# Optimization experiments

Measured on AMD Instinct MI355X. Metric: run time of the kernel, lower is better.

Reference implementation:

```python
import jax, jax.numpy as jnp
import numpy as np

# Static problem dims (match input_specs / init_kwargs)
B, NQ, C, H = 2, 900, 256, 8
HGT, WID = 64, 64            # single-scale feature map (input_spatial_shapes = [[64, 64]])
N = HGT * WID                # 4096 keys
DH = C // H                  # head dim 32
RPE_HID = 512
STRIDE = 16                  # feature_stride


def setup_inputs() -> dict:
    key = jax.random.key(0)
    ks = jax.random.split(key, 24)
    p = lambda k, shape: jax.random.normal(k, shape, jnp.float32) * 0.02
    # reference boxes (cx, cy, w, h) in pixel coords of a 1024x1024 image
    ref = jax.random.uniform(ks[0], (B, NQ, 1, 4), jnp.float32)
    ref = jnp.concatenate([ref[..., :2] * (WID * STRIDE), ref[..., 2:] * 128.0], axis=-1)
    return {
        "vggt_features": jnp.zeros((1,), jnp.float32),  # unused by forward (kept for signature fidelity)
        "query": jax.random.normal(ks[1], (B, NQ, C), jnp.float32),
        "reference_2d": ref,
        "k_input_flatten": jax.random.normal(ks[2], (B, N, C), jnp.float32),
        "v_input_flatten": jax.random.normal(ks[3], (B, N, C), jnp.float32),
        "input_spatial_shapes": jnp.array([[HGT, WID]], jnp.int32),
        "input_padding_mask": jnp.zeros((B, N), jnp.bool_),
        # cpb_mlp1 (x) and cpb_mlp2 (y): Linear(2,512)+ReLU+Linear(512,H,no bias); stored as [in,out]
        "W1x": p(ks[4], (2, RPE_HID)), "b1x": jnp.zeros((RPE_HID,), jnp.float32), "W2x": p(ks[5], (RPE_HID, H)),
        "W1y": p(ks[6], (2, RPE_HID)), "b1y": jnp.zeros((RPE_HID,), jnp.float32), "W2y": p(ks[7], (RPE_HID, H)),
        "Wq": p(ks[8], (C, C)), "bq": jnp.zeros((C,), jnp.float32),
        "Wk": p(ks[9], (C, C)), "bk": jnp.zeros((C,), jnp.float32),
        "Wv": p(ks[10], (C, C)), "bv": jnp.zeros((C,), jnp.float32),
        "Wp": p(ks[11], (C, C)), "bp": jnp.zeros((C,), jnp.float32),
    }


def _mlp(d, W1, b1, W2):
    return jax.nn.relu(d @ W1 + b1) @ W2


def reference(vggt_features, query, reference_2d, k_input_flatten, v_input_flatten,
              input_spatial_shapes, input_padding_mask,
              W1x, b1x, W2x, W1y, b1y, W2y, Wq, bq, Wk, bk, Wv, bv, Wp, bp):
    h, w = HGT, WID  # static (input_spatial_shapes[0] == [HGT, WID])
    scale = DH ** -0.5
    # cxcywh -> xyxy: [B, NQ, 1, 4]
    xyxy = jnp.concatenate([reference_2d[..., :2] - reference_2d[..., 2:] / 2,
                            reference_2d[..., :2] + reference_2d[..., 2:] / 2], axis=-1)
    # pixel-center grid coords (linspace(0.5, w-0.5, w) * stride)
    pos_x = ((jnp.arange(w, dtype=jnp.float32) + 0.5) * STRIDE)[None, None, :, None]
    pos_y = ((jnp.arange(h, dtype=jnp.float32) + 0.5) * STRIDE)[None, None, :, None]
    delta_x = xyxy[..., 0::2] - pos_x  # [B, NQ, w, 2]  (x1, x2 rel. to columns)
    delta_y = xyxy[..., 1::2] - pos_y  # [B, NQ, h, 2]  (y1, y2 rel. to rows)
    rpe_x = _mlp(delta_x, W1x, b1x, W2x)  # [B, NQ, w, H]
    rpe_y = _mlp(delta_y, W1y, b1y, W2y)  # [B, NQ, h, H]
    # broadcast add over (row, col) then flatten spatial -> [B, H, NQ, N]
    rpe = (rpe_x[:, :, None] + rpe_y[:, :, :, None]).reshape(B, NQ, h * w, H).transpose(0, 3, 1, 2)
    q = (query @ Wq + bq).reshape(B, NQ, H, DH).transpose(0, 2, 1, 3) * scale  # [B,H,NQ,DH]
    k = (k_input_flatten @ Wk + bk).reshape(B, N, H, DH).transpose(0, 2, 1, 3)  # [B,H,N,DH]
    v = (v_input_flatten @ Wv + bv).reshape(B, N, H, DH).transpose(0, 2, 1, 3)  # [B,H,N,DH]
    attn = jnp.einsum('bhqd,bhkd->bhqk', q, k) + rpe
    attn = attn + input_padding_mask[:, None, None, :].astype(attn.dtype) * (-100.0)
    # torch.clip_ to finfo(min,max) is an identity on finite values; softmax follows
    attn = jax.nn.softmax(attn, axis=-1)
    x = jnp.einsum('bhqk,bhkd->bhqd', attn, v).transpose(0, 2, 1, 3).reshape(B, NQ, C)
    return x @ Wp + bp
```

## Files before the change

kernel.cpp:

```cpp
#include <hip/hip_runtime.h>
#include <hip/hip_bf16.h>
#include <cmath>

#define B_ 2
#define NQ_ 900
#define N_ 4096
#define LOG2E 1.4426950408889634f

typedef __attribute__((ext_vector_type(4))) float f32x4;
typedef __attribute__((ext_vector_type(8))) short s16x8;
typedef __attribute__((ext_vector_type(8))) _Float16 f16x8;

__device__ inline short f2bf(float x) {
    union { __hip_bfloat16 b; short s; } u;
    u.b = __float2bfloat16(x);
    return u.s;
}
__device__ inline short f2h(float x) {
    _Float16 h = (_Float16)x;
    return __builtin_bit_cast(short, h);
}

template <int CTRL>
__device__ inline float dppf(float x) {
    int xi = __builtin_bit_cast(int, x);
    int r = __builtin_amdgcn_update_dpp(xi, xi, CTRL, 0xF, 0xF, true);
    return __builtin_bit_cast(float, r);
}
__device__ inline float rowmax16(float v) {
    v = fmaxf(v, dppf<0x121>(v));
    v = fmaxf(v, dppf<0x122>(v));
    v = fmaxf(v, dppf<0x124>(v));
    v = fmaxf(v, dppf<0x128>(v));
    return v;
}
__device__ inline float rowsum16(float v) {
    v += dppf<0x121>(v);
    v += dppf<0x122>(v);
    v += dppf<0x124>(v);
    v += dppf<0x128>(v);
    return v;
}

__global__ __launch_bounds__(256) void stage1_kernel(
    const float* __restrict__ query, const float* __restrict__ kin,
    const float* __restrict__ vin,
    const float* __restrict__ Wq, const float* __restrict__ Wk,
    const float* __restrict__ Wv,
    const float* __restrict__ bqv, const float* __restrict__ bkv,
    const float* __restrict__ bvv,
    unsigned short* __restrict__ qbf, unsigned short* __restrict__ kbf,
    unsigned short* __restrict__ vbf, float qscale,
    const float* __restrict__ ref2d,
    const float* __restrict__ W1x, const float* __restrict__ b1x,
    const float* __restrict__ W1y, const float* __restrict__ b1y,
    const float* __restrict__ W2x, const float* __restrict__ W2y,
    float* __restrict__ rpe_x, float* __restrict__ rpe_y)
{
    __shared__ uint4 smem[3072];
    const int bx = blockIdx.x;
    const int tid = threadIdx.x;
    const int w = tid >> 6, l = tid & 63, quad = l >> 4, l15 = l & 15;

    if (bx < 285) {
        short* Ab = (short*)smem;
        short* Bb = (short*)smem + 16384;
        const int mtx = bx < 29 ? 0 : (bx < 157 ? 1 : 2);
        const int tile = bx - (mtx == 0 ? 0 : mtx == 1 ? 29 : 157);
        const int m0 = tile * 64;
        const float* X = mtx == 0 ? query : mtx == 1 ? kin : vin;
        const float* W = mtx == 0 ? Wq : mtx == 1 ? Wk : Wv;
        const float* bias = mtx == 0 ? bqv : mtx == 1 ? bkv : bvv;
        unsigned short* Y = mtx == 0 ? qbf : mtx == 1 ? kbf : vbf;
        const int M = mtx == 0 ? 1800 : 8192;
        const float alpha = mtx == 0 ? qscale : 1.0f;
        const int rows_per_b = mtx == 0 ? 900 : 4096;
        const int ROWS = mtx == 0 ? 960 : 4096;
        const int wq = tid & 3, mm = tid >> 2;

        {
            const bool valid = (m0 + mm) < M;
            const float* xr = X + (size_t)(m0 + mm) * 256;
            #pragma unroll
            for (int it = 0; it < 8; ++it) {
                int g2 = it * 4 + wq;
                float4 a0 = make_float4(0.f, 0.f, 0.f, 0.f), a1 = a0;
                if (valid) {
                    a0 = *(const float4*)(xr + g2 * 8);
                    a1 = *(const float4*)(xr + g2 * 8 + 4);
                }
                uint4 pk;
                pk.x = (unsigned)(unsigned short)f2bf(a0.x) | ((unsigned)(unsigned short)f2bf(a0.y) << 16);
                pk.y = (unsigned)(unsigned short)f2bf(a0.z) | ((unsigned)(unsigned short)f2bf(a0.w) << 16);
                pk.z = (unsigned)(unsigned short)f2bf(a1.x) | ((unsigned)(unsigned short)f2bf(a1.y) << 16);
                pk.w = (unsigned)(unsigned short)f2bf(a1.z) | ((unsigned)(unsigned short)f2bf(a1.w) << 16);
                *(uint4*)(Ab + (it * 256 + mm * 4 + wq) * 8) = pk;
            }
        }

        for (int nt0 = 0; nt0 < 4; ++nt0) {
            const int n0 = nt0 * 64;
            f32x4 acc[4] = {{0.f,0.f,0.f,0.f},{0.f,0.f,0.f,0.f},{0.f,0.f,0.f,0.f},{0.f,0.f,0.f,0.f}};
            for (int kh = 0; kh < 2; ++kh) {
                {
                    const float* wcol = W + n0 + mm;
                    #pragma unroll
                    for (int it = 0; it < 4; ++it) {
                        int g2 = it * 4 + wq;
                        int kb = kh * 128 + g2 * 8;
                        uint4 wk4;
                        wk4.x = (unsigned)(unsigned short)f2bf(wcol[(kb + 0) * 256])
                              | ((unsigned)(unsigned short)f2bf(wcol[(kb + 1) * 256]) << 16);
                        wk4.y = (unsigned)(unsigned short)f2bf(wcol[(kb + 2) * 256])
                              | ((unsigned)(unsigned short)f2bf(wcol[(kb + 3) * 256]) << 16);
                        wk4.z = (unsigned)(unsigned short)f2bf(wcol[(kb + 4) * 256])
                              | ((unsigned)(unsigned short)f2bf(wcol[(kb + 5) * 256]) << 16);
                        wk4.w = (unsigned)(unsigned short)f2bf(wcol[(kb + 6) * 256])
                              | ((unsigned)(unsigned short)f2bf(wcol[(kb + 7) * 256]) << 16);
                        *(uint4*)(Bb + (it * 256 + mm * 4 + wq) * 8) = wk4;
                    }
                }
                __syncthreads();

                #pragma unroll
                for (int kc = 0; kc < 4; ++kc) {
                    int kcg = kh * 4 + kc;
                    s16x8 a = *(const s16x8*)(Ab + (kcg * 256 + (w * 16 + l15) * 4 + quad) * 8);
                    #pragma unroll
                    for (int nt = 0; nt < 4; ++nt) {
                        s16x8 bf = *(const s16x8*)(Bb + (kc * 256 + (nt * 16 + l15) * 4 + quad) * 8);
                        acc[nt] = __builtin_amdgcn_mfma_f32_16x16x32_bf16(a, bf, acc[nt], 0, 0, 0);
                    }
                }
                __syncthreads();
            }

            #pragma unroll
            for (int nt = 0; nt < 4; ++nt) {
                int n = n0 + nt * 16 + l15;
                float bs = bias[n];
                int h = n >> 5, d = n & 31;
                #pragma unroll
                for (int r = 0; r < 4; ++r) {
                    int row = m0 + w * 16 + quad * 4 + r;
                    if (row < M) {
                        int b = row / rows_per_b;
                        int pos = row - b * rows_per_b;
                        Y[((size_t)(b * 8 + h) * ROWS + pos) * 32 + d] =
                            (unsigned short)f2bf((acc[nt][r] + bs) * alpha);
                    }
                }
            }
        }
    } else {
        short* sw2h = (short*)smem;
        short* sw2l = (short*)smem + 8192;
        float4* sUV = (float4*)(smem + 2048);
        const int bq = bx - 285;

        for (int i = tid; i < 8192; i += 256) {
            int g = i >> 3, j = i & 7;
            int kcg = g >> 6, rr = g & 63, n = rr >> 2, q4 = rr & 3;
            int k = kcg * 32 + q4 * 8 + j;
            float val = ((n < 8) ? W2x[k * 8 + n] : W2y[k * 8 + (n - 8)]) * LOG2E;
            _Float16 hi = (_Float16)val;
            sw2h[i] = __builtin_bit_cast(short, hi);
            sw2l[i] = f2h(val - (float)hi);
        }
        for (int k = tid; k < 512; k += 256) {
            float w1x0 = W1x[k], w1x1 = W1x[512 + k];
            float w1y0 = W1y[k], w1y1 = W1y[512 + k];
            float bxv = b1x[k], byv = b1y[k];
            float vx = -(w1x0 + w1x1), vy = -(w1y0 + w1y1);
            const float4 bb = *(const float4*)(ref2d + (size_t)bq * 4);
            float ux = fmaf(w1x0, bb.x - bb.z * 0.5f, fmaf(w1x1, bb.x + bb.z * 0.5f, bxv));
            float uy = fmaf(w1y0, bb.y - bb.w * 0.5f, fmaf(w1y1, bb.y + bb.w * 0.5f, byv));
            sUV[(k >> 3) * 9 + (k & 7)] = make_float4(ux, vx, uy, vy);
        }

        const int wrow = w;
        const int row = wrow * 16 + l15;
        const float pc = (row + 0.5f) * 16.0f;

        __syncthreads();

        f32x4 accx = {0.f, 0.f, 0.f, 0.f}, accy = {0.f, 0.f, 0.f, 0.f};
        for (int kc = 0; kc < 16; ++kc) {
            f16x8 axh, axl, ayh, ayl;
            #pragma unroll
            for (int i = 0; i < 8; ++i) {
                float4 u = sUV[(kc * 4 + quad) * 9 + i];
                float hx = fmaxf(fmaf(u.y, pc, u.x), 0.f);
                float hy = fmaxf(fmaf(u.w, pc, u.z), 0.f);
                _Float16 xh = (_Float16)hx;
                _Float16 yh = (_Float16)hy;
                axh[i] = xh;
                axl[i] = (_Float16)(hx - (float)xh);
                ayh[i] = yh;
                ayl[i] = (_Float16)(hy - (float)yh);
            }
            f16x8 bh = *(const f16x8*)(sw2h + (kc * 64 + l15 * 4 + quad) * 8);
            f16x8 bl = *(const f16x8*)(sw2l + (kc * 64 + l15 * 4 + quad) * 8);
            accx = __builtin_amdgcn_mfma_f32_16x16x32_f16(axh, bh, accx, 0, 0, 0);
            accx = __builtin_amdgcn_mfma_f32_16x16x32_f16(axh, bl, accx, 0, 0, 0);
            accx = __builtin_amdgcn_mfma_f32_16x16x32_f16(axl, bh, accx, 0, 0, 0);
            accy = __builtin_amdgcn_mfma_f32_16x16x32_f16(ayh, bh, accy, 0, 0, 0);
            accy = __builtin_amdgcn_mfma_f32_16x16x32_f16(ayh, bl, accy, 0, 0, 0);
            accy = __builtin_amdgcn_mfma_f32_16x16x32_f16(ayl, bh, accy, 0, 0, 0);
        }

        #pragma unroll
        for (int rr = 0; rr < 4; ++rr) {
            int row_out = wrow * 16 + quad * 4 + rr;
            if (l15 < 8) rpe_x[((size_t)l15 * 1800 + bq) * 64 + row_out] = accx[rr];
            else         rpe_y[((size_t)(l15 - 8) * 1800 + bq) * 64 + row_out] = accy[rr];
        }
    }
}

__global__ __launch_bounds__(256) void outproj_kernel(
    const float* __restrict__ X, const float* __restrict__ W,
    const float* __restrict__ bias, float* __restrict__ Y, int M)
{
    __shared__ short Abh[4096], Abl[4096], Bbh[4096], Bbl[4096];
    const int tid = threadIdx.x;
    const int m0 = blockIdx.x * 64, n0 = blockIdx.y * 64;
    const int w = tid >> 6, l = tid & 63, quad = l >> 4, l15 = l & 15;
    const int wq = tid & 3, mm = tid >> 2;
    const bool valid = (m0 + mm) < M;
    const float* xr = X + (size_t)(m0 + mm) * 256;
    const float* wcol = W + n0 + mm;

    f32x4 acc[4] = {{0.f,0.f,0.f,0.f},{0.f,0.f,0.f,0.f},{0.f,0.f,0.f,0.f},{0.f,0.f,0.f,0.f}};

    for (int kq = 0; kq < 4; ++kq) {
        #pragma unroll
        for (int it = 0; it < 2; ++it) {
            int g2 = it * 4 + wq;
            int kbase = kq * 64 + g2 * 8;
            float av[8], bv[8];
            #pragma unroll
            for (int j = 0; j < 8; ++j) {
                av[j] = valid ? xr[kbase + j] : 0.f;
                bv[j] = wcol[(kbase + j) * 256];
            }
            uint4 ah, al, bh, bl;
            unsigned* ahp = (unsigned*)&ah; unsigned* alp = (unsigned*)&al;
            unsigned* bhp = (unsigned*)&bh; unsigned* blp = (unsigned*)&bl;
            #pragma unroll
            for (int j2 = 0; j2 < 4; ++j2) {
                _Float16 h0 = (_Float16)av[j2 * 2], h1 = (_Float16)av[j2 * 2 + 1];
                ahp[j2] = (unsigned)(unsigned short)__builtin_bit_cast(short, h0)
                        | ((unsigned)(unsigned short)__builtin_bit_cast(short, h1) << 16);
                alp[j2] = (unsigned)(unsigned short)f2h(av[j2 * 2] - (float)h0)
                        | ((unsigned)(unsigned short)f2h(av[j2 * 2 + 1] - (float)h1) << 16);
                _Float16 g0 = (_Float16)bv[j2 * 2], g1 = (_Float16)bv[j2 * 2 + 1];
                bhp[j2] = (unsigned)(unsigned short)__builtin_bit_cast(short, g0)
                        | ((unsigned)(unsigned short)__builtin_bit_cast(short, g1) << 16);
                blp[j2] = (unsigned)(unsigned short)f2h(bv[j2 * 2] - (float)g0)
                        | ((unsigned)(unsigned short)f2h(bv[j2 * 2 + 1] - (float)g1) << 16);
            }
            int gi = (it * 256 + mm * 4 + wq) * 8;
            *(uint4*)(Abh + gi) = ah;
            *(uint4*)(Abl + gi) = al;
            *(uint4*)(Bbh + gi) = bh;
            *(uint4*)(Bbl + gi) = bl;
        }
        __syncthreads();

        #pragma unroll
        for (int kc = 0; kc < 2; ++kc) {
            int ga = (kc * 256 + (w * 16 + l15) * 4 + quad) * 8;
            f16x8 ah = *(const f16x8*)(Abh + ga);
            f16x8 al = *(const f16x8*)(Abl + ga);
            #pragma unroll
            for (int nt = 0; nt < 4; ++nt) {
                int gb = (kc * 256 + (nt * 16 + l15) * 4 + quad) * 8;
                f16x8 bh = *(const f16x8*)(Bbh + gb);
                f16x8 bl = *(const f16x8*)(Bbl + gb);
                acc[nt] = __builtin_amdgcn_mfma_f32_16x16x32_f16(ah, bh, acc[nt], 0, 0, 0);
                acc[nt] = __builtin_amdgcn_mfma_f32_16x16x32_f16(ah, bl, acc[nt], 0, 0, 0);
                acc[nt] = __builtin_amdgcn_mfma_f32_16x16x32_f16(al, bh, acc[nt], 0, 0, 0);
            }
        }
        __syncthreads();
    }

    #pragma unroll
    for (int nt = 0; nt < 4; ++nt) {
        int n = n0 + nt * 16 + l15;
        float bs = bias[n];
        #pragma unroll
        for (int r = 0; r < 4; ++r) {
            int row = m0 + w * 16 + quad * 4 + r;
            if (row < M)
                Y[(size_t)row * 256 + n] = acc[nt][r] + bs;
        }
    }
}

__global__ __launch_bounds__(512, 4) void attn_mfma_kernel(
    const unsigned short* __restrict__ qb16, const unsigned short* __restrict__ kb16,
    const unsigned short* __restrict__ vb16,
    const float* __restrict__ rpe_x, const float* __restrict__ rpe_y,
    const unsigned char* __restrict__ mask, float* __restrict__ xout)
{
    __shared__ short skf[4 * 2048];
    __shared__ short svt[4 * 2048];
    __shared__ short spb[8 * 544];
    __shared__ float ry[32 * 65];
    __shared__ unsigned long long smaskb[64];
    __shared__ float sm[8][16], sl[8][16], sLf[32];

    const int tid = threadIdx.x;
    const int qb = blockIdx.x, h = blockIdx.y, b = blockIdx.z;
    const int q0 = qb * 32;
    const int w = tid >> 6, l = tid & 63;
    const int qsub = w >> 2, g = w & 3;
    const int quad = l >> 4, l15 = l & 15;

    const unsigned short* qg = qb16 + (size_t)(b * 8 + h) * 960 * 32;
    const unsigned short* kg = kb16 + (size_t)(b * 8 + h) * 4096 * 32;
    const unsigned short* vg = vb16 + (size_t)(b * 8 + h) * 4096 * 32;
    const float* rxh = rpe_x + ((size_t)h * 1800 + b * NQ_) * 64;
    const float* ryh = rpe_y + ((size_t)h * 1800 + b * NQ_) * 64;

    for (int i = tid; i < 2048; i += 512) {
        int qq = q0 + (i >> 6), pos = i & 63;
        float vy = 0.f;
        if (qq < NQ_)
            vy = ryh[(size_t)qq * 64 + pos];
        ry[(i >> 6) * 65 + pos] = vy;
    }
    #pragma unroll
    for (int j = 0; j < 8; ++j) {
        int c = w * 8 + j;
        unsigned long long bits = __ballot(mask[(size_t)b * N_ + c * 64 + l] != 0);
        if (l == 0) smaskb[c] = bits;
    }

    s16x8 qa = *(const s16x8*)(qg + (size_t)(q0 + qsub * 16 + l15) * 32 + quad * 8);

    f32x4 rx4[4];
    #pragma unroll
    for (int t = 0; t < 4; ++t)
        #pragma unroll
        for (int r = 0; r < 4; ++r) {
            int qq = q0 + qsub * 16 + quad * 4 + r;
            rx4[t][r] = (qq < NQ_) ? rxh[(size_t)qq * 64 + t * 16 + l15] : 0.f;
        }

    const int sg = tid >> 7, role = (tid >> 6) & 1, stl = tid & 63;
    int eoff[4];
    if (role == 0) {
        #pragma unroll
        for (int t = 0; t < 4; ++t)
            eoff[t] = (t * 16 + (stl & 15)) * 32 + (stl >> 4) * 8;
    } else {
        #pragma unroll
        for (int t = 0; t < 4; ++t)
            eoff[t] = stl * 32 + t * 8;
    }
    const unsigned short* src = role ? vg : kg;

    uint4 pf[4];
    {
        size_t cb = (size_t)(sg * 16) * 2048;
        #pragma unroll
        for (int t = 0; t < 4; ++t) pf[t] = *(const uint4*)(src + cb + eoff[t]);
    }

    float mrow[4] = {-INFINITY, -INFINITY, -INFINITY, -INFINITY};
    float lrow[4] = {0.f, 0.f, 0.f, 0.f};
    f32x4 acc0 = {0.f, 0.f, 0.f, 0.f}, acc1 = {0.f, 0.f, 0.f, 0.f};
    short* pw = spb + w * 544;

    for (int i = 0; i < 16; ++i) {
        __syncthreads();
        if (role == 0) {
            #pragma unroll
            for (int t = 0; t < 4; ++t)
                *(uint4*)(skf + sg * 2048 + (t * 64 + stl) * 8) = pf[t];
        } else {
            short* vtw = svt + sg * 2048;
            #pragma unroll
            for (int t = 0; t < 4; ++t) {
                const unsigned short* pv = (const unsigned short*)&pf[t];
                #pragma unroll
                for (int j = 0; j < 8; ++j) {
                    int d = t * 8 + j;
                    vtw[d * 64 + (((stl >> 3) ^ (d & 7)) << 3) + (stl & 7)] = (short)pv[j];
                }
            }
        }
        __syncthreads();

        {
            int inext = (i + 1 < 16) ? i + 1 : 15;
            size_t cb = (size_t)(sg * 16 + inext) * 2048;
            #pragma unroll
            for (int t = 0; t < 4; ++t) pf[t] = *(const uint4*)(src + cb + eoff[t]);
        }

        const int cgc = g * 16 + i;
        const short* kf = skf + g * 2048;

        f32x4 sc[4];
        #pragma unroll
        for (int t = 0; t < 4; ++t) {
            s16x8 kb = *(const s16x8*)(kf + (t * 64 + l) * 8);
            sc[t] = __builtin_amdgcn_mfma_f32_16x16x32_bf16(qa, kb, rx4[t], 0, 0, 0);
        }
        float ryv[4];
        #pragma unroll
        for (int r = 0; r < 4; ++r)
            ryv[r] = ry[(qsub * 16 + quad * 4 + r) * 65 + cgc];
        unsigned long long mb = smaskb[cgc];
        if (mb) {
            #pragma unroll
            for (int t = 0; t < 4; ++t) {
                float mk = ((mb >> (t * 16 + l15)) & 1ULL) ? -144.2695f : 0.f;
                #pragma unroll
                for (int r = 0; r < 4; ++r) sc[t][r] += mk;
            }
        }

        float cmr[4];
        #pragma unroll
        for (int r = 0; r < 4; ++r)
            cmr[r] = fmaxf(fmaxf(sc[0][r], sc[1][r]), fmaxf(sc[2][r], sc[3][r])) + ryv[r];

        int ok = (cmr[0] <= mrow[0] + 8.f) & (cmr[1] <= mrow[1] + 8.f)
               & (cmr[2] <= mrow[2] + 8.f) & (cmr[3] <= mrow[3] + 8.f);
        if (!__all(ok)) {
            #pragma unroll
            for (int r = 0; r < 4; ++r) {
                float cm = rowmax16(cmr[r]);
                float mnew = fmaxf(mrow[r], cm);
                float al = exp2f(mrow[r] - mnew);
                mrow[r] = mnew;
                lrow[r] *= al;
                acc0[r] *= al;
                acc1[r] *= al;
            }
        }

        float msub[4];
        #pragma unroll
        for (int r = 0; r < 4; ++r) msub[r] = mrow[r] - ryv[r];
        #pragma unroll
        for (int t = 0; t < 4; ++t)
            #pragma unroll
            for (int r = 0; r < 4; ++r)
                sc[t][r] = exp2f(sc[t][r] - msub[r]);
        #pragma unroll
        for (int r = 0; r < 4; ++r)
            lrow[r] += (sc[0][r] + sc[1][r]) + (sc[2][r] + sc[3][r]);

        const short* vt = svt + g * 2048;
        #pragma unroll
        for (int hh = 0; hh < 2; ++hh) {
            #pragma unroll
            for (int tt = 0; tt < 2; ++tt) {
                int t = hh * 2 + tt;
                int gphys = (tt * 2 + (l15 >> 3)) ^ quad;
                #pragma unroll
                for (int r = 0; r < 4; ++r)
                    pw[(gphys * 17 + quad * 4 + r) * 8 + (l15 & 7)] = f2bf(sc[t][r]);
            }
            int gph_r = quad ^ (l15 >> 2);
            s16x8 pa  = *(const s16x8*)(pw + (gph_r * 17 + l15) * 8);
            int ksw = ((hh * 4 + quad) ^ (l15 & 7)) * 8;
            s16x8 vb0 = *(const s16x8*)(vt + l15 * 64 + ksw);
            s16x8 vb1 = *(const s16x8*)(vt + (16 + l15) * 64 + ksw);
            acc0 = __builtin_amdgcn_mfma_f32_16x16x32_bf16(pa, vb0, acc0, 0, 0, 0);
            acc1 = __builtin_amdgcn_mfma_f32_16x16x32_bf16(pa, vb1, acc1, 0, 0, 0);
        }
    }

    #pragma unroll
    for (int r = 0; r < 4; ++r) lrow[r] = rowsum16(lrow[r]);

    __syncthreads();
    if (l15 == 0) {
        #pragma unroll
        for (int r = 0; r < 4; ++r) {
            sm[w][quad * 4 + r] = mrow[r];
            sl[w][quad * 4 + r] = lrow[r];
        }
    }
    __syncthreads();
    float wgt[4], L4[4];
    #pragma unroll
    for (int r = 0; r < 4; ++r) {
        int qrow = quad * 4 + r;
        float mm = -INFINITY;
        #pragma unroll
        for (int gg = 0; gg < 4; ++gg) mm = fmaxf(mm, sm[qsub * 4 + gg][qrow]);
        float LL = 0.f;
        #pragma unroll
        for (int gg = 0; gg < 4; ++gg)
            LL += exp2f(sm[qsub * 4 + gg][qrow] - mm) * sl[qsub * 4 + gg][qrow];
        wgt[r] = exp2f(mrow[r] - mm);
        L4[r] = LL;
    }
    if (g == 0 && l15 == 0) {
        #pragma unroll
        for (int r = 0; r < 4; ++r) sLf[qsub * 16 + quad * 4 + r] = L4[r];
    }

    float* obuf = (float*)skf;
    for (int gg = 0; gg < 4; ++gg) {
        if (g == gg) {
            #pragma unroll
            for (int r = 0; r < 4; ++r) {
                int idx = (qsub * 16 + quad * 4 + r) * 33 + l15;
                float v0 = wgt[r] * acc0[r];
                float v1 = wgt[r] * acc1[r];
                if (gg == 0) { obuf[idx] = v0; obuf[idx + 16] = v1; }
                else         { obuf[idx] += v0; obuf[idx + 16] += v1; }
            }
        }
        __syncthreads();
    }

    for (int i = tid; i < 1024; i += 512) {
        int ql = i >> 5, d = i & 31;
        int qq = q0 + ql;
        if (qq < NQ_)
            xout[(size_t)(b * NQ_ + qq) * 256 + h * 32 + d] = obuf[ql * 33 + d] / sLf[ql];
    }
}

extern "C" void kernel_launch(void* const* d_in, const int* in_sizes, int n_in,
                              void* d_out, int out_size, void* d_ws, size_t ws_size,
                              hipStream_t stream)
{
    const float* query = (const float*)d_in[1];
    const float* ref2d = (const float*)d_in[2];
    const float* kin   = (const float*)d_in[3];
    const float* vin   = (const float*)d_in[4];
    const unsigned char* mask = (const unsigned char*)d_in[6];
    const float* W1x = (const float*)d_in[7];
    const float* b1x = (const float*)d_in[8];
    const float* W2x = (const float*)d_in[9];
    const float* W1y = (const float*)d_in[10];
    const float* b1y = (const float*)d_in[11];
    const float* W2y = (const float*)d_in[12];
    const float* Wq  = (const float*)d_in[13];
    const float* bq  = (const float*)d_in[14];
    const float* Wk  = (const float*)d_in[15];
    const float* bk  = (const float*)d_in[16];
    const float* Wv  = (const float*)d_in[17];
    const float* bv  = (const float*)d_in[18];
    const float* Wp  = (const float*)d_in[19];
    const float* bp  = (const float*)d_in[20];

    char* wsb = (char*)d_ws;
    unsigned short* qbf = (unsigned short*)(wsb);
    unsigned short* kbf = (unsigned short*)(wsb +   983040);
    unsigned short* vbf = (unsigned short*)(wsb +  5177344);
    float* rxws = (float*)(wsb +  9371648);
    float* ryws = (float*)(wsb + 13058048);
    float* xws  = (float*)(wsb + 16744448);
    float* out  = (float*)d_out;

    const float qscale = LOG2E / sqrtf(32.0f);

    stage1_kernel<<<2085, 256, 0, stream>>>(
        query, kin, vin, Wq, Wk, Wv, bq, bk, bv, qbf, kbf, vbf, qscale,
        ref2d, W1x, b1x, W1y, b1y, W2x, W2y, rxws, ryws);
    attn_mfma_kernel<<<dim3(29, 8, B_), 512, 0, stream>>>(
        qbf, kbf, vbf, rxws, ryws, mask, xws);
    outproj_kernel<<<dim3(29, 4), 256, 0, stream>>>(xws, Wp, bp, out, 1800);
}
```

Measured before the change: 218.0 us.

## Keep GEMM A-fragments in registers and batch four queries per RPE block

The projection GEMM path now loads each wave's A rows straight into register fragments instead of staging them in shared memory. The full 256-deep weight slice is staged once per n-tile, which removes the K-half split and one barrier pair. The RPE path processes four queries per block, reusing the staged W2 hi/lo tables and W1 values, so the grid shrinks from 2085 to 735 blocks. The costs are higher register pressure and a serialized per-query loop with extra barriers inside each RPE block.

Measured after the change: 203.9 us. 1.07x faster.

```diff
diff --git a/kernel.cpp b/kernel.cpp
--- a/kernel.cpp
+++ b/kernel.cpp
@@ -57,14 +57,13 @@
     const float* __restrict__ W2x, const float* __restrict__ W2y,
     float* __restrict__ rpe_x, float* __restrict__ rpe_y)
 {
-    __shared__ uint4 smem[3072];
+    __shared__ uint4 smem[2560];
     const int bx = blockIdx.x;
     const int tid = threadIdx.x;
     const int w = tid >> 6, l = tid & 63, quad = l >> 4, l15 = l & 15;
 
     if (bx < 285) {
-        short* Ab = (short*)smem;
-        short* Bb = (short*)smem + 16384;
+        short* Bb = (short*)smem;
         const int mtx = bx < 29 ? 0 : (bx < 157 ? 1 : 2);
         const int tile = bx - (mtx == 0 ? 0 : mtx == 1 ? 29 : 157);
         const int m0 = tile * 64;
@@ -78,61 +77,56 @@
         const int ROWS = mtx == 0 ? 960 : 4096;
         const int wq = tid & 3, mm = tid >> 2;
 
+        s16x8 afr[8];
         {
-            const bool valid = (m0 + mm) < M;
-            const float* xr = X + (size_t)(m0 + mm) * 256;
-            #pragma unroll
-            for (int it = 0; it < 8; ++it) {
-                int g2 = it * 4 + wq;
+            const int arow = m0 + w * 16 + l15;
+            const bool avalid = arow < M;
+            const float* xr = X + (size_t)arow * 256;
+            #pragma unroll
+            for (int kc = 0; kc < 8; ++kc) {
                 float4 a0 = make_float4(0.f, 0.f, 0.f, 0.f), a1 = a0;
-                if (valid) {
-                    a0 = *(const float4*)(xr + g2 * 8);
-                    a1 = *(const float4*)(xr + g2 * 8 + 4);
+                if (avalid) {
+                    a0 = *(const float4*)(xr + kc * 32 + quad * 8);
+                    a1 = *(const float4*)(xr + kc * 32 + quad * 8 + 4);
                 }
-                uint4 pk;
-                pk.x = (unsigned)(unsigned short)f2bf(a0.x) | ((unsigned)(unsigned short)f2bf(a0.y) << 16);
-                pk.y = (unsigned)(unsigned short)f2bf(a0.z) | ((unsigned)(unsigned short)f2bf(a0.w) << 16);
-                pk.z = (unsigned)(unsigned short)f2bf(a1.x) | ((unsigned)(unsigned short)f2bf(a1.y) << 16);
-                pk.w = (unsigned)(unsigned short)f2bf(a1.z) | ((unsigned)(unsigned short)f2bf(a1.w) << 16);
-                *(uint4*)(Ab + (it * 256 + mm * 4 + wq) * 8) = pk;
+                unsigned pk0 = (unsigned)(unsigned short)f2bf(a0.x) | ((unsigned)(unsigned short)f2bf(a0.y) << 16);
+                unsigned pk1 = (unsigned)(unsigned short)f2bf(a0.z) | ((unsigned)(unsigned short)f2bf(a0.w) << 16);
+                unsigned pk2 = (unsigned)(unsigned short)f2bf(a1.x) | ((unsigned)(unsigned short)f2bf(a1.y) << 16);
+                unsigned pk3 = (unsigned)(unsigned short)f2bf(a1.z) | ((unsigned)(unsigned short)f2bf(a1.w) << 16);
+                uint4 pk = make_uint4(pk0, pk1, pk2, pk3);
+                afr[kc] = __builtin_bit_cast(s16x8, pk);
             }
         }
 
         for (int nt0 = 0; nt0 < 4; ++nt0) {
             const int n0 = nt0 * 64;
+            {
+                const float* wcol = W + n0 + mm;
+                #pragma unroll
+                for (int it = 0; it < 8; ++it) {
+                    int g2 = it * 4 + wq;
+                    uint4 wk4;
+                    wk4.x = (unsigned)(unsigned short)f2bf(wcol[(g2 * 8 + 0) * 256])
+                          | ((unsigned)(unsigned short)f2bf(wcol[(g2 * 8 + 1) * 256]) << 16);
+                    wk4.y = (unsigned)(unsigned short)f2bf(wcol[(g2 * 8 + 2) * 256])
+                          | ((unsigned)(unsigned short)f2bf(wcol[(g2 * 8 + 3) * 256]) << 16);
+                    wk4.z = (unsigned)(unsigned short)f2bf(wcol[(g2 * 8 + 4) * 256])
+                          | ((unsigned)(unsigned short)f2bf(wcol[(g2 * 8 + 5) * 256]) << 16);
+                    wk4.w = (unsigned)(unsigned short)f2bf(wcol[(g2 * 8 + 6) * 256])
+                          | ((unsigned)(unsigned short)f2bf(wcol[(g2 * 8 + 7) * 256]) << 16);
+                    *(uint4*)(Bb + (it * 256 + mm * 4 + wq) * 8) = wk4;
+                }
+            }
+            __syncthreads();
+
             f32x4 acc[4] = {{0.f,0.f,0.f,0.f},{0.f,0.f,0.f,0.f},{0.f,0.f,0.f,0.f},{0.f,0.f,0.f,0.f}};
-            for (int kh = 0; kh < 2; ++kh) {
-                {
-                    const float* wcol = W + n0 + mm;
-                    #pragma unroll
-                    for (int it = 0; it < 4; ++it) {
-                        int g2 = it * 4 + wq;
-                        int kb = kh * 128 + g2 * 8;
-                        uint4 wk4;
-                        wk4.x = (unsigned)(unsigned short)f2bf(wcol[(kb + 0) * 256])
-                              | ((unsigned)(unsigned short)f2bf(wcol[(kb + 1) * 256]) << 16);
-                        wk4.y = (unsigned)(unsigned short)f2bf(wcol[(kb + 2) * 256])
-                              | ((unsigned)(unsigned short)f2bf(wcol[(kb + 3) * 256]) << 16);
-                        wk4.z = (unsigned)(unsigned short)f2bf(wcol[(kb + 4) * 256])
-                              | ((unsigned)(unsigned short)f2bf(wcol[(kb + 5) * 256]) << 16);
-                        wk4.w = (unsigned)(unsigned short)f2bf(wcol[(kb + 6) * 256])
-                              | ((unsigned)(unsigned short)f2bf(wcol[(kb + 7) * 256]) << 16);
-                        *(uint4*)(Bb + (it * 256 + mm * 4 + wq) * 8) = wk4;
-                    }
+            #pragma unroll
+            for (int kc = 0; kc < 8; ++kc) {
+                #pragma unroll
+                for (int nt = 0; nt < 4; ++nt) {
+                    s16x8 bf = *(const s16x8*)(Bb + (kc * 256 + (nt * 16 + l15) * 4 + quad) * 8);
+                    acc[nt] = __builtin_amdgcn_mfma_f32_16x16x32_bf16(afr[kc], bf, acc[nt], 0, 0, 0);
                 }
-                __syncthreads();
-
-                #pragma unroll
-                for (int kc = 0; kc < 4; ++kc) {
-                    int kcg = kh * 4 + kc;
-                    s16x8 a = *(const s16x8*)(Ab + (kcg * 256 + (w * 16 + l15) * 4 + quad) * 8);
-                    #pragma unroll
-                    for (int nt = 0; nt < 4; ++nt) {
-                        s16x8 bf = *(const s16x8*)(Bb + (kc * 256 + (nt * 16 + l15) * 4 + quad) * 8);
-                        acc[nt] = __builtin_amdgcn_mfma_f32_16x16x32_bf16(a, bf, acc[nt], 0, 0, 0);
-                    }
-                }
-                __syncthreads();
             }
 
             #pragma unroll
@@ -151,12 +145,13 @@
                     }
                 }
             }
+            __syncthreads();
         }
     } else {
         short* sw2h = (short*)smem;
         short* sw2l = (short*)smem + 8192;
         float4* sUV = (float4*)(smem + 2048);
-        const int bq = bx - 285;
+        const int bq0 = (bx - 285) * 4;
 
         for (int i = tid; i < 8192; i += 256) {
             int g = i >> 3, j = i & 7;
@@ -167,53 +162,66 @@
             sw2h[i] = __builtin_bit_cast(short, hi);
             sw2l[i] = f2h(val - (float)hi);
         }
-        for (int k = tid; k < 512; k += 256) {
-            float w1x0 = W1x[k], w1x1 = W1x[512 + k];
-            float w1y0 = W1y[k], w1y1 = W1y[512 + k];
-            float bxv = b1x[k], byv = b1y[k];
-            float vx = -(w1x0 + w1x1), vy = -(w1y0 + w1y1);
-            const float4 bb = *(const float4*)(ref2d + (size_t)bq * 4);
-            float ux = fmaf(w1x0, bb.x - bb.z * 0.5f, fmaf(w1x1, bb.x + bb.z * 0.5f, bxv));
-            float uy = fmaf(w1y0, bb.y - bb.w * 0.5f, fmaf(w1y1, bb.y + bb.w * 0.5f, byv));
-            sUV[(k >> 3) * 9 + (k & 7)] = make_float4(ux, vx, uy, vy);
-        }
+
+        const int k0 = tid, k1 = tid + 256;
+        const float w1x0a = W1x[k0], w1x1a = W1x[512 + k0];
+        const float w1y0a = W1y[k0], w1y1a = W1y[512 + k0];
+        const float bxa = b1x[k0], bya = b1y[k0];
+        const float vxa = -(w1x0a + w1x1a), vya = -(w1y0a + w1y1a);
+        const float w1x0b = W1x[k1], w1x1b = W1x[512 + k1];
+        const float w1y0b = W1y[k1], w1y1b = W1y[512 + k1];
+        const float bxb = b1x[k1], byb = b1y[k1];
+        const float vxb = -(w1x0b + w1x1b), vyb = -(w1y0b + w1y1b);
 
         const int wrow = w;
         const int row = wrow * 16 + l15;
         const float pc = (row + 0.5f) * 16.0f;
 
-        __syncthreads();
-
-        f32x4 accx = {0.f, 0.f, 0.f, 0.f}, accy = {0.f, 0.f, 0.f, 0.f};
-        for (int kc = 0; kc < 16; ++kc) {
-            f16x8 axh, axl, ayh, ayl;
-            #pragma unroll
-            for (int i = 0; i < 8; ++i) {
-                float4 u = sUV[(kc * 4 + quad) * 9 + i];
-                float hx = fmaxf(fmaf(u.y, pc, u.x), 0.f);
-                float hy = fmaxf(fmaf(u.w, pc, u.z), 0.f);
-                _Float16 xh = (_Float16)hx;
-                _Float16 yh = (_Float16)hy;
-                axh[i] = xh;
-                axl[i] = (_Float16)(hx - (float)xh);
-                ayh[i] = yh;
-                ayl[i] = (_Float16)(hy - (float)yh);
-            }
-            f16x8 bh = *(const f16x8*)(sw2h + (kc * 64 + l15 * 4 + quad) * 8);
-            f16x8 bl = *(const f16x8*)(sw2l + (kc * 64 + l15 * 4 + quad) * 8);
-            accx = __builtin_amdgcn_mfma_f32_16x16x32_f16(axh, bh, accx, 0, 0, 0);
-            accx = __builtin_amdgcn_mfma_f32_16x16x32_f16(axh, bl, accx, 0, 0, 0);
-            accx = __builtin_amdgcn_mfma_f32_16x16x32_f16(axl, bh, accx, 0, 0, 0);
-            accy = __builtin_amdgcn_mfma_f32_16x16x32_f16(ayh, bh, accy, 0, 0, 0);
-            accy = __builtin_amdgcn_mfma_f32_16x16x32_f16(ayh, bl, accy, 0, 0, 0);
-            accy = __builtin_amdgcn_mfma_f32_16x16x32_f16(ayl, bh, accy, 0, 0, 0);
-        }
-
-        #pragma unroll
-        for (int rr = 0; rr < 4; ++rr) {
-            int row_out = wrow * 16 + quad * 4 + rr;
-            if (l15 < 8) rpe_x[((size_t)l15 * 1800 + bq) * 64 + row_out] = accx[rr];
-            else         rpe_y[((size_t)(l15 - 8) * 1800 + bq) * 64 + row_out] = accy[rr];
+        for (int qi = 0; qi < 4; ++qi) {
+            const int bq = bq0 + qi;
+            {
+                const float4 bb = *(const float4*)(ref2d + (size_t)bq * 4);
+                float x1 = bb.x - bb.z * 0.5f, x2 = bb.x + bb.z * 0.5f;
+                float y1 = bb.y - bb.w * 0.5f, y2 = bb.y + bb.w * 0.5f;
+                sUV[k0] = make_float4(fmaf(w1x0a, x1, fmaf(w1x1a, x2, bxa)), vxa,
+                                      fmaf(w1y0a, y1, fmaf(w1y1a, y2, bya)), vya);
+                sUV[k1] = make_float4(fmaf(w1x0b, x1, fmaf(w1x1b, x2, bxb)), vxb,
+                                      fmaf(w1y0b, y1, fmaf(w1y1b, y2, byb)), vyb);
+            }
+            __syncthreads();
+
+            f32x4 accx = {0.f, 0.f, 0.f, 0.f}, accy = {0.f, 0.f, 0.f, 0.f};
+            for (int kc = 0; kc < 16; ++kc) {
+                f16x8 axh, axl, ayh, ayl;
+                #pragma unroll
+                for (int i = 0; i < 8; ++i) {
+                    float4 u = sUV[kc * 32 + quad * 8 + i];
+                    float hx = fmaxf(fmaf(u.y, pc, u.x), 0.f);
+                    float hy = fmaxf(fmaf(u.w, pc, u.z), 0.f);
+                    _Float16 xh = (_Float16)hx;
+                    _Float16 yh = (_Float16)hy;
+                    axh[i] = xh;
+                    axl[i] = (_Float16)(hx - (float)xh);
+                    ayh[i] = yh;
+                    ayl[i] = (_Float16)(hy - (float)yh);
+                }
+                f16x8 bh = *(const f16x8*)(sw2h + (kc * 64 + l15 * 4 + quad) * 8);
+                f16x8 bl = *(const f16x8*)(sw2l + (kc * 64 + l15 * 4 + quad) * 8);
+                accx = __builtin_amdgcn_mfma_f32_16x16x32_f16(axh, bh, accx, 0, 0, 0);
+                accx = __builtin_amdgcn_mfma_f32_16x16x32_f16(axh, bl, accx, 0, 0, 0);
+                accx = __builtin_amdgcn_mfma_f32_16x16x32_f16(axl, bh, accx, 0, 0, 0);
+                accy = __builtin_amdgcn_mfma_f32_16x16x32_f16(ayh, bh, accy, 0, 0, 0);
+                accy = __builtin_amdgcn_mfma_f32_16x16x32_f16(ayh, bl, accy, 0, 0, 0);
+                accy = __builtin_amdgcn_mfma_f32_16x16x32_f16(ayl, bh, accy, 0, 0, 0);
+            }
+
+            #pragma unroll
+            for (int rr = 0; rr < 4; ++rr) {
+                int row_out = wrow * 16 + quad * 4 + rr;
+                if (l15 < 8) rpe_x[((size_t)l15 * 1800 + bq) * 64 + row_out] = accx[rr];
+                else         rpe_y[((size_t)(l15 - 8) * 1800 + bq) * 64 + row_out] = accy[rr];
+            }
+            __syncthreads();
         }
     }
 }
@@ -567,7 +575,7 @@
 
     const float qscale = LOG2E / sqrtf(32.0f);
 
-    stage1_kernel<<<2085, 256, 0, stream>>>(
+    stage1_kernel<<<735, 256, 0, stream>>>(
         query, kin, vin, Wq, Wk, Wv, bq, bk, bv, qbf, kbf, vbf, qscale,
         ref2d, W1x, b1x, W1y, b1y, W2x, W2y, rxws, ryws);
     attn_mfma_kernel<<<dim3(29, 8, B_), 512, 0, stream>>>(
```
